# Optimization experiments

Hardware: AMD Instinct MI355X
Metric: run time of the kernel (lower is better)

## Reference

```python
import jax, jax.numpy as jnp
import numpy as np

C = 1024
D = C // 8      # query/key channels
R = C // 16     # channel-attention reduction
B, H, W = 4, 64, 64


def setup_inputs() -> dict:
    key = jax.random.key(0)
    ks = jax.random.split(key, 10)
    s = lambda k, shp, fan: jax.random.normal(k, shp, jnp.float32) * (1.0 / np.sqrt(fan))
    return {
        "x": jax.random.normal(ks[0], (B, C, H, W), jnp.float32),
        "x1": jax.random.normal(ks[1], (B, C, H, W), jnp.float32),
        "Wq": s(ks[2], (D, C), C), "bq": jnp.zeros((D,), jnp.float32),
        "Wk": s(ks[3], (D, C), C), "bk": jnp.zeros((D,), jnp.float32),
        "Wv": s(ks[4], (C, C), C), "bv": jnp.zeros((C,), jnp.float32),
        "Wca1": s(ks[5], (R, C), C),  # CBAM MLP, no bias
        "Wca2": s(ks[6], (C, R), R),
    }


def _forward(x, x1, Wq, bq, Wk, bk, Wv, bv, Wca1, Wca2):
    b, c, h, w = x.shape
    n = h * w
    # 1x1 convs as channel matmuls
    Q = (jnp.einsum('bchw,dc->bdhw', x, Wq) + bq[:, None, None]).reshape(b, D, n)   # [B,D,N]
    K = (jnp.einsum('bchw,dc->bdhw', x, Wk) + bk[:, None, None]).reshape(b, D, n)   # [B,D,N]
    V = (jnp.einsum('bchw,oc->bohw', x1, Wv) + bv[:, None, None]).reshape(b, c, n)  # [B,C,N]
    # energy[b,n,m] = Q[:,n] . K[:,m]
    energy = jnp.einsum('bdn,bdm->bnm', Q, K)
    att = jax.nn.sigmoid(energy)                       # [B,N,N]
    # torch: bmm(V, att^T) -> out[b,c,n] = sum_m V[b,c,m] * att[b,n,m]
    out = jnp.einsum('bcm,bnm->bcn', V, att).reshape(b, c, h, w)
    # ChannelAttention (CBAM): shared MLP on avg+max pooled features, sigmoid gate
    avg = out.mean(axis=(2, 3))                        # [B,C]
    mx = out.max(axis=(2, 3))                          # [B,C]
    mlp = lambda v: jnp.einsum('cr,br->bc', Wca2, jax.nn.relu(jnp.einsum('rc,bc->br', Wca1, v)))
    gate = jax.nn.sigmoid(mlp(avg) + mlp(mx))          # [B,C]
    return out * gate[:, :, None, None]


def reference(x, x1, Wq, bq, Wk, bk, Wv, bv, Wca1, Wca2):
    return _forward(x, x1, Wq, bq, Wk, bk, Wv, bv, Wca1, Wca2)
```

## Files before the change

### kernel.cpp

```cpp
#include <hip/hip_runtime.h>
#include <hip/hip_fp16.h>
#include <cstdint>

typedef _Float16 f16;
typedef __attribute__((ext_vector_type(8))) _Float16 half8;
typedef __attribute__((ext_vector_type(4))) float floatx4;
typedef __attribute__((ext_vector_type(16))) float floatx16;

#define CC 1024
#define DD 128
#define RRR 64
#define BBATCH 4
#define NNN 4096

#define BM 128
#define BN 128
#define BK 64

__device__ __forceinline__ void gl_lds16(const void* g, void* l) {
  __builtin_amdgcn_global_load_lds(
      (__attribute__((address_space(1))) void*)(uintptr_t)g,
      (__attribute__((address_space(3))) void*)l, 16, 0, 0);
}

template<int EPI>
__global__ __launch_bounds__(256)
void gemm_bt(const f16* __restrict__ A, const f16* __restrict__ Bp, f16* __restrict__ Cout,
             const float* __restrict__ bias, int N, int K,
             int lda, int ldb, int ldc, size_t sA, size_t sB, size_t sC)
{
  __shared__ __align__(16) f16 S[2 * BM * BK];
  f16* As = S;
  f16* Bs = S + BM * BK;

  const int z = blockIdx.z;
  const int tid  = threadIdx.x;
  const int lane = tid & 63;
  const int wave = tid >> 6;
  const int m0 = blockIdx.y * BM;
  const int n0 = blockIdx.x * BN;
  const int wm = (wave >> 1) * 64;
  const int wn = (wave & 1) * 64;
  const int l31 = lane & 31;
  const int hi  = lane >> 5;
  const int rs  = lane & 7;

  const f16* Ab = A  + (size_t)z * sA + (size_t)m0 * lda;
  const f16* Bb = Bp + (size_t)z * sB + (size_t)n0 * ldb;

  floatx16 acc[2][2];
#pragma unroll
  for (int i = 0; i < 2; ++i)
#pragma unroll
    for (int j = 0; j < 2; ++j)
#pragma unroll
      for (int r = 0; r < 16; ++r)
        acc[i][j][r] = 0.f;

  int srow[4], ssrc[4];
#pragma unroll
  for (int r = 0; r < 4; ++r) {
    const int gi = r * 256 + tid;
    const int row = gi >> 3;
    const int gc  = gi & 7;
    srow[r] = row;
    ssrc[r] = ((gc ^ (row & 7)) << 3);
  }

  for (int k0 = 0; k0 < K; k0 += BK) {
#pragma unroll
    for (int r = 0; r < 4; ++r) {
      gl_lds16(Ab + (size_t)srow[r] * lda + k0 + ssrc[r], As + (size_t)(r * 256 + tid) * 8);
      gl_lds16(Bb + (size_t)srow[r] * ldb + k0 + ssrc[r], Bs + (size_t)(r * 256 + tid) * 8);
    }
    __syncthreads();

#pragma unroll
    for (int kk = 0; kk < BK; kk += 16) {
      const int gr = (((kk >> 3) + hi) ^ rs) << 3;
      half8 af[2], bfr[2];
#pragma unroll
      for (int i = 0; i < 2; ++i)
        af[i] = *(const half8*)(As + (wm + i * 32 + l31) * BK + gr);
#pragma unroll
      for (int j = 0; j < 2; ++j)
        bfr[j] = *(const half8*)(Bs + (wn + j * 32 + l31) * BK + gr);
#pragma unroll
      for (int i = 0; i < 2; ++i)
#pragma unroll
        for (int j = 0; j < 2; ++j)
          acc[i][j] = __builtin_amdgcn_mfma_f32_32x32x16_f16(af[i], bfr[j], acc[i][j], 0, 0, 0);
    }
    __syncthreads();
  }

  f16* Ch = Cout + (size_t)z * sC;
  f16* Ct = S;
#pragma unroll
  for (int i = 0; i < 2; ++i)
#pragma unroll
    for (int j = 0; j < 2; ++j)
#pragma unroll
      for (int r = 0; r < 16; ++r) {
        const int rl = wm + i * 32 + (r & 3) + 8 * (r >> 2) + 4 * hi;
        const int cl = wn + j * 32 + l31;
        const float v = acc[i][j][r];
        f16 h;
        if constexpr (EPI == 0)      h = (f16)v;
        else if constexpr (EPI == 1) h = (f16)(v + bias[m0 + rl]);
        else if constexpr (EPI == 2) h = (f16)(v + bias[n0 + cl]);
        else                         h = (f16)(1.0f / (1.0f + __expf(-v)));
        Ct[rl * BN + ((((cl >> 3) ^ (rl & 7)) << 3) | (cl & 7))] = h;
      }
  __syncthreads();
#pragma unroll
  for (int p = 0; p < 8; ++p) {
    const int idx = p * 256 + tid;
    const int rl = idx >> 4;
    const int g  = idx & 15;
    half8 vv = *(const half8*)(Ct + rl * BN + ((g ^ (rl & 7)) << 3));
    *(half8*)(Ch + (size_t)(m0 + rl) * ldc + n0 + g * 8) = vv;
  }
}

#define G8_STAGE(MATG, MIDX, LD, H, KT, BUF) do {                                   \
    gl_lds16(MATG + (size_t)((H) * 128 + srow) * (LD) + (KT) * 64 + soff,           \
             &S[BUF][MIDX][(H) * 8192 + tid * 8]);                                  \
    gl_lds16(MATG + (size_t)((H) * 128 + 64 + srow) * (LD) + (KT) * 64 + soff,      \
             &S[BUF][MIDX][(H) * 8192 + 4096 + tid * 8]);                           \
  } while (0)

#define G8_LDA(DST, MA) do {                                                        \
    _Pragma("unroll") for (int ms = 0; ms < 4; ++ms)                                \
    _Pragma("unroll") for (int ks = 0; ks < 2; ++ks)                                \
      DST[ms * 2 + ks] = *(const half8*)(Ac + aRow + (MA) * 4096 + ms * 1024 + sws[ks]); \
  } while (0)

#define G8_LDB(NH) do {                                                             \
    _Pragma("unroll") for (int ns = 0; ns < 2; ++ns)                                \
    _Pragma("unroll") for (int ks = 0; ks < 2; ++ks)                                \
      bf[NH][ns * 2 + ks] = *(const half8*)(Bc + bRow + (NH) * 2048 + ns * 1024 + sws[ks]); \
  } while (0)

#define G8_MFMA(SRC, MA, NH) do {                                                   \
    __builtin_amdgcn_s_setprio(1);                                                  \
    _Pragma("unroll") for (int ms = 0; ms < 4; ++ms)                                \
    _Pragma("unroll") for (int ns = 0; ns < 2; ++ns)                                \
    _Pragma("unroll") for (int ks = 0; ks < 2; ++ks)                                \
      acc[(MA) * 4 + ms][(NH) * 2 + ns] = __builtin_amdgcn_mfma_f32_16x16x32_f16(   \
          SRC[ms * 2 + ks], bf[NH][ns * 2 + ks], acc[(MA) * 4 + ms][(NH) * 2 + ns], 0, 0, 0); \
    __builtin_amdgcn_s_setprio(0);                                                  \
  } while (0)

template<int EPI>
__global__ __launch_bounds__(512, 2)
void gemm8p(const f16* __restrict__ A, const f16* __restrict__ Bp, f16* __restrict__ Cout,
            const float* __restrict__ bias, int K,
            int lda, int ldb, int ldc, size_t sA, size_t sB, size_t sC)
{
  __shared__ __align__(16) f16 S[2][2][16384];

  const int tid  = threadIdx.x;
  const int lane = tid & 63;
  const int wave = tid >> 6;
  const int wm   = wave >> 2;
  const int wn   = wave & 3;
  const int l15  = lane & 15;
  const int lk   = lane >> 4;
  const int z    = blockIdx.z;
  const int m0   = blockIdx.y * 256;
  const int n0   = blockIdx.x * 256;

  const f16* Ag = A  + (size_t)z * sA + (size_t)m0 * lda;
  const f16* Bg = Bp + (size_t)z * sB + (size_t)n0 * ldb;

  const int srow = tid >> 3;
  const int soff = (((tid & 7) ^ (srow & 7)) << 3);

  int sws[2];
#pragma unroll
  for (int ks = 0; ks < 2; ++ks) sws[ks] = (((ks * 4 + lk) ^ (l15 & 7)) << 3);
  const int aRow = (wm * 128 + l15) * 64;
  const int bRow = (wn * 64 + l15) * 64;

  floatx4 acc[8][4];
#pragma unroll
  for (int i = 0; i < 8; ++i)
#pragma unroll
    for (int j = 0; j < 4; ++j)
#pragma unroll
      for (int r = 0; r < 4; ++r) acc[i][j][r] = 0.f;

  half8 af[8], a2[8], bf[2][4];

  const int NT = K >> 6;

  G8_STAGE(Ag, 0, lda, 0, 0, 0);
  G8_STAGE(Bg, 1, ldb, 0, 0, 0);
  G8_STAGE(Ag, 0, lda, 1, 0, 0);
  G8_STAGE(Bg, 1, ldb, 1, 0, 0);
  if (NT > 1) {
    G8_STAGE(Ag, 0, lda, 0, 1, 1);
    G8_STAGE(Bg, 1, ldb, 0, 1, 1);
    G8_STAGE(Ag, 0, lda, 1, 1, 1);
    G8_STAGE(Bg, 1, ldb, 1, 1, 1);
    asm volatile("s_waitcnt vmcnt(8)" ::: "memory");
  } else {
    asm volatile("s_waitcnt vmcnt(0)" ::: "memory");
  }
  __builtin_amdgcn_s_barrier();
  __builtin_amdgcn_sched_barrier(0);

  for (int t = 0; t < NT; ++t) {
    const int cur = t & 1;
    const f16* Ac = &S[cur][0][0];
    const f16* Bc = &S[cur][1][0];

    G8_LDA(af, 0); G8_LDB(0); G8_LDB(1);
    G8_MFMA(af, 0, 0);
    G8_LDA(a2, 1);
    G8_MFMA(af, 0, 1);
    G8_MFMA(a2, 1, 1);
    G8_MFMA(a2, 1, 0);

    asm volatile("s_waitcnt lgkmcnt(0)" ::: "memory");
    __builtin_amdgcn_s_barrier();
    __builtin_amdgcn_sched_barrier(0);

    if (t + 2 < NT) {
      G8_STAGE(Ag, 0, lda, 0, t + 2, cur);
      G8_STAGE(Bg, 1, ldb, 0, t + 2, cur);
      G8_STAGE(Ag, 0, lda, 1, t + 2, cur);
      G8_STAGE(Bg, 1, ldb, 1, t + 2, cur);
      asm volatile("s_waitcnt vmcnt(8)" ::: "memory");
      __builtin_amdgcn_s_barrier();
      __builtin_amdgcn_sched_barrier(0);
    } else if (t + 1 < NT) {
      asm volatile("s_waitcnt vmcnt(0)" ::: "memory");
      __builtin_amdgcn_s_barrier();
      __builtin_amdgcn_sched_barrier(0);
    }
  }

  f16* Ct = &S[0][0][0];
  f16* Ch = Cout + (size_t)z * sC;
#pragma unroll
  for (int mi = 0; mi < 8; ++mi)
#pragma unroll
    for (int ni = 0; ni < 4; ++ni)
#pragma unroll
      for (int r = 0; r < 4; ++r) {
        const int rl = wm * 128 + mi * 16 + lk * 4 + r;
        const int cl = wn * 64 + ni * 16 + l15;
        const float v = acc[mi][ni][r];
        f16 h;
        if constexpr (EPI == 1)      h = (f16)(v + bias[m0 + rl]);
        else if constexpr (EPI == 3) h = (f16)(1.0f / (1.0f + __expf(-v)));
        else                         h = (f16)v;
        Ct[rl * 256 + ((((cl >> 3) ^ (rl & 7)) << 3) | (cl & 7))] = h;
      }
  asm volatile("s_waitcnt lgkmcnt(0)" ::: "memory");
  __builtin_amdgcn_s_barrier();
#pragma unroll
  for (int p = 0; p < 16; ++p) {
    const int idx = p * 512 + tid;
    const int rl = idx >> 5;
    const int g  = idx & 31;
    half8 vv = *(const half8*)(Ct + rl * 256 + ((g ^ (rl & 7)) << 3));
    *(half8*)(Ch + (size_t)(m0 + rl) * ldc + n0 + g * 8) = vv;
  }
}

#undef G8_STAGE
#undef G8_LDA
#undef G8_LDB
#undef G8_MFMA

__global__ __launch_bounds__(256)
void prep(const float* __restrict__ Wq, const float* __restrict__ Wk, const float* __restrict__ Wv,
          const float* __restrict__ bq, const float* __restrict__ bk,
          f16* __restrict__ WQKb, f16* __restrict__ Wvb, float* __restrict__ bqk)
{
  const int NV = CC * CC;
  const int NQ = DD * CC;
  int i = blockIdx.x * 256 + threadIdx.x;
  if (i < NV)                    Wvb[i] = (f16)Wv[i];
  else if (i < NV + NQ)          WQKb[i - NV] = (f16)Wq[i - NV];
  else if (i < NV + 2 * NQ)      WQKb[i - NV] = (f16)Wk[i - NV - NQ];
  else if (i < NV + 2 * NQ + 2 * DD) {
    int t = i - NV - 2 * NQ;
    bqk[t] = (t < DD) ? bq[t] : bk[t - DD];
  }
}

__global__ __launch_bounds__(256)
void transpose_cvt(const float* __restrict__ x, const float* __restrict__ x1,
                   f16* __restrict__ ox, f16* __restrict__ ox1, int nb)
{
  const int zz = blockIdx.z;
  const int b  = (zz < nb) ? zz : zz - nb;
  const float* in = ((zz < nb) ? x : x1) + (size_t)b * CC * NNN;
  f16* out = ((zz < nb) ? ox : ox1) + (size_t)b * CC * NNN;
  __shared__ float tile[64][65];
  const int c0 = blockIdx.y * 64;
  const int n0 = blockIdx.x * 64;
  const int t  = threadIdx.x;
  const int rn = (t & 15) * 4;
  const int rc = t >> 4;
#pragma unroll
  for (int r = 0; r < 4; ++r) {
    const float4 v = *(const float4*)(in + (size_t)(c0 + rc + r * 16) * NNN + n0 + rn);
    tile[rc + r * 16][rn]     = v.x;
    tile[rc + r * 16][rn + 1] = v.y;
    tile[rc + r * 16][rn + 2] = v.z;
    tile[rc + r * 16][rn + 3] = v.w;
  }
  __syncthreads();
  const int ce = (t & 7) * 8;
  const int nr = t >> 3;
#pragma unroll
  for (int r = 0; r < 2; ++r) {
    half8 vv;
#pragma unroll
    for (int e = 0; e < 8; ++e) vv[e] = (f16)tile[ce + e][nr + r * 32];
    *(half8*)(out + (size_t)(n0 + nr + r * 32) * CC + c0 + ce) = vv;
  }
}

__global__ __launch_bounds__(256)
void rowreduce(const f16* __restrict__ X, float* __restrict__ avg, float* __restrict__ mx, int ncols)
{
  const size_t ridx = (size_t)blockIdx.y * gridDim.x + blockIdx.x;
  const half8* p = (const half8*)(X + ridx * ncols);
  float s = 0.f, m = -3.402823466e38f;
  for (int i = threadIdx.x; i < ncols / 8; i += 256) {
    half8 v = p[i];
#pragma unroll
    for (int e = 0; e < 8; ++e) {
      float f = (float)v[e];
      s += f;
      m = fmaxf(m, f);
    }
  }
#pragma unroll
  for (int o = 32; o > 0; o >>= 1) {
    s += __shfl_down(s, o);
    m = fmaxf(m, __shfl_down(m, o));
  }
  __shared__ float ss[4], sm[4];
  if ((threadIdx.x & 63) == 0) { ss[threadIdx.x >> 6] = s; sm[threadIdx.x >> 6] = m; }
  __syncthreads();
  if (threadIdx.x == 0) {
    s = ss[0] + ss[1] + ss[2] + ss[3];
    m = fmaxf(fmaxf(sm[0], sm[1]), fmaxf(sm[2], sm[3]));
    avg[ridx] = s / (float)ncols;
    mx[ridx] = m;
  }
}

__global__ __launch_bounds__(256)
void mlp_gate(const float* __restrict__ avg, const float* __restrict__ mxv,
              const float* __restrict__ W1, const float* __restrict__ W2,
              float* __restrict__ gate)
{
  const int z = blockIdx.x;
  avg += (size_t)z * CC; mxv += (size_t)z * CC; gate += (size_t)z * CC;
  const int t = threadIdx.x;
  const int r = t & 63;
  const int part = t >> 6;
  __shared__ float pa[4][64], pm[4][64], h[RRR];
  {
    const float* w = W1 + (size_t)r * CC + part * 256;
    const float* av = avg + part * 256;
    const float* mv = mxv + part * 256;
    float sa = 0.f, sm = 0.f;
    for (int c = 0; c < 256; ++c) { float wv = w[c]; sa += wv * av[c]; sm += wv * mv[c]; }
    pa[part][r] = sa; pm[part][r] = sm;
  }
  __syncthreads();
  if (t < RRR) {
    float A_ = pa[0][t] + pa[1][t] + pa[2][t] + pa[3][t];
    float M_ = pm[0][t] + pm[1][t] + pm[2][t] + pm[3][t];
    h[t] = fmaxf(A_, 0.f) + fmaxf(M_, 0.f);
  }
  __syncthreads();
  for (int c = t; c < CC; c += 256) {
    float s = 0.f;
    for (int rr = 0; rr < RRR; ++rr) s += W2[(size_t)c * RRR + rr] * h[rr];
    gate[c] = 1.0f / (1.0f + __expf(-s));
  }
}

__global__ __launch_bounds__(256)
void scale_out(const f16* __restrict__ oh, float* __restrict__ out, const float* __restrict__ gate)
{
  oh  += (size_t)blockIdx.y * CC * NNN;
  out += (size_t)blockIdx.y * CC * NNN;
  gate += (size_t)blockIdx.y * CC;
  size_t i = (size_t)blockIdx.x * 256 + threadIdx.x;
  half8 v = ((const half8*)oh)[i];
  const float g = gate[(i * 8) >> 12];
  float4 a = { (float)v[0] * g, (float)v[1] * g, (float)v[2] * g, (float)v[3] * g };
  float4 b = { (float)v[4] * g, (float)v[5] * g, (float)v[6] * g, (float)v[7] * g };
  float4* o = (float4*)out;
  o[2 * i]     = a;
  o[2 * i + 1] = b;
}

extern "C" void kernel_launch(void* const* d_in, const int* in_sizes, int n_in,
                              void* d_out, int out_size, void* d_ws, size_t ws_size,
                              hipStream_t stream)
{
  const float* x    = (const float*)d_in[0];
  const float* x1   = (const float*)d_in[1];
  const float* Wq   = (const float*)d_in[2];
  const float* bq   = (const float*)d_in[3];
  const float* Wk   = (const float*)d_in[4];
  const float* bk   = (const float*)d_in[5];
  const float* Wv   = (const float*)d_in[6];
  const float* bv   = (const float*)d_in[7];
  const float* Wca1 = (const float*)d_in[8];
  const float* Wca2 = (const float*)d_in[9];
  float* out = (float*)d_out;

  char* ws = (char*)d_ws;
  size_t off = 0;
  auto alloc = [&](size_t bytes) { void* p = ws + off; off += (bytes + 255) & ~255ULL; return p; };

  f16* WQKb = (f16*)alloc((size_t)2 * DD * CC * 2);
  f16* Wvb  = (f16*)alloc((size_t)CC * CC * 2);
  float* bqk  = (float*)alloc(256 * 4);
  float* avg  = (float*)alloc((size_t)BBATCH * CC * 4);
  float* mxv  = (float*)alloc((size_t)BBATCH * CC * 4);
  float* gate = (float*)alloc((size_t)BBATCH * CC * 4);

  const size_t attB = (size_t)NNN * NNN * 2;
  const size_t xTB  = (size_t)BBATCH * NNN * CC * 2;
  const size_t qkB  = (size_t)BBATCH * NNN * 2 * DD * 2;
  const size_t vBB  = (size_t)BBATCH * CC * NNN * 2;
  const size_t ohB  = (size_t)BBATCH * CC * NNN * 2;
  const size_t fixedEnd = off;

  const dim3 blk(256);
  const int prepN = CC * CC + 2 * DD * CC + 2 * DD;
  prep<<<(prepN + 255) / 256, blk, 0, stream>>>(Wq, Wk, Wv, bq, bk, WQKb, Wvb, bqk);

  {
    size_t offF = fixedEnd;
    auto af_ = [&](size_t bytes) { void* p = ws + offF; offF += (bytes + 255) & ~255ULL; return p; };
    f16* QKt  = (f16*)af_(qkB);
    f16* Vb   = (f16*)af_(vBB);
    f16* outh = (f16*)af_(ohB);
    f16* att  = (f16*)af_((size_t)BBATCH * attB);
    if (offF + (1 << 20) <= ws_size) {
      f16* xTb  = att;
      f16* x1Tb = att + (size_t)BBATCH * NNN * CC;

      transpose_cvt<<<dim3(NNN / 64, CC / 64, 2 * BBATCH), blk, 0, stream>>>(x, x1, xTb, x1Tb, BBATCH);

      gemm_bt<2><<<dim3(2 * DD / BN, NNN / BM, BBATCH), blk, 0, stream>>>(
          xTb, WQKb, QKt, bqk, 2 * DD, CC,
          CC, CC, 2 * DD, (size_t)NNN * CC, 0, (size_t)NNN * 2 * DD);
      gemm8p<1><<<dim3(NNN / 256, CC / 256, BBATCH), dim3(512), 0, stream>>>(
          Wvb, x1Tb, Vb, bv, CC,
          CC, CC, NNN, 0, (size_t)NNN * CC, (size_t)CC * NNN);

      const size_t sQK = (size_t)NNN * 2 * DD;
      gemm8p<3><<<dim3(NNN / 256, NNN / 256, BBATCH), dim3(512), 0, stream>>>(
          QKt, QKt + DD, att, nullptr, DD,
          2 * DD, 2 * DD, NNN, sQK, sQK, (size_t)NNN * NNN);
      gemm8p<0><<<dim3(NNN / 256, CC / 256, BBATCH), dim3(512), 0, stream>>>(
          Vb, att, outh, nullptr, NNN,
          NNN, NNN, NNN, (size_t)CC * NNN, (size_t)NNN * NNN, (size_t)CC * NNN);

      rowreduce<<<dim3(CC, BBATCH), blk, 0, stream>>>(outh, avg, mxv, NNN);
      mlp_gate<<<BBATCH, blk, 0, stream>>>(avg, mxv, Wca1, Wca2, gate);
      scale_out<<<dim3(CC * NNN / 8 / 256, BBATCH), blk, 0, stream>>>(outh, out, gate);
      return;
    }
  }

  int g = 0;
  for (int cand = BBATCH; cand >= 1; cand >>= 1) {
    size_t need = fixedEnd + 2 * xTB + qkB + vBB + ohB + (size_t)cand * attB + (1 << 20);
    if (need <= ws_size) { g = cand; break; }
  }

  if (g > 0) {
    f16* xTb  = (f16*)alloc(xTB);
    f16* x1Tb = (f16*)alloc(xTB);
    f16* QKt  = (f16*)alloc(qkB);
    f16* Vb   = (f16*)alloc(vBB);
    f16* outh = (f16*)alloc(ohB);
    f16* att  = (f16*)alloc((size_t)g * attB);

    transpose_cvt<<<dim3(NNN / 64, CC / 64, 2 * BBATCH), blk, 0, stream>>>(x, x1, xTb, x1Tb, BBATCH);

    gemm_bt<2><<<dim3(2 * DD / BN, NNN / BM, BBATCH), blk, 0, stream>>>(
        xTb, WQKb, QKt, bqk, 2 * DD, CC,
        CC, CC, 2 * DD, (size_t)NNN * CC, 0, (size_t)NNN * 2 * DD);
    gemm_bt<1><<<dim3(NNN / BN, CC / BM, BBATCH), blk, 0, stream>>>(
        Wvb, x1Tb, Vb, bv, NNN, CC,
        CC, CC, NNN, 0, (size_t)NNN * CC, (size_t)CC * NNN);

    for (int b0 = 0; b0 < BBATCH; b0 += g) {
      const int gc = (b0 + g <= BBATCH) ? g : (BBATCH - b0);
      const size_t sQK = (size_t)NNN * 2 * DD;
      gemm_bt<3><<<dim3(NNN / BN, NNN / BM, gc), blk, 0, stream>>>(
          QKt + (size_t)b0 * sQK, QKt + (size_t)b0 * sQK + DD, att, nullptr,
          NNN, DD, 2 * DD, 2 * DD, NNN, sQK, sQK, (size_t)NNN * NNN);
      gemm_bt<0><<<dim3(NNN / BN, CC / BM, gc), blk, 0, stream>>>(
          Vb + (size_t)b0 * CC * NNN, att, outh + (size_t)b0 * CC * NNN, nullptr,
          NNN, NNN, NNN, NNN, NNN,
          (size_t)CC * NNN, (size_t)NNN * NNN, (size_t)CC * NNN);
    }

    rowreduce<<<dim3(CC, BBATCH), blk, 0, stream>>>(outh, avg, mxv, NNN);
    mlp_gate<<<BBATCH, blk, 0, stream>>>(avg, mxv, Wca1, Wca2, gate);
    scale_out<<<dim3(CC * NNN / 8 / 256, BBATCH), blk, 0, stream>>>(outh, out, gate);
  } else {
    f16* xTb  = (f16*)alloc((size_t)NNN * CC * 2);
    f16* x1Tb = (f16*)alloc((size_t)NNN * CC * 2);
    f16* QKt  = (f16*)alloc((size_t)NNN * 2 * DD * 2);
    f16* Vb   = (f16*)alloc((size_t)CC * NNN * 2);
    f16* outh = (f16*)alloc((size_t)CC * NNN * 2);
    f16* att  = (f16*)alloc(attB);

    for (int b = 0; b < BBATCH; ++b) {
      const float* xb  = x  + (size_t)b * CC * NNN;
      const float* x1b = x1 + (size_t)b * CC * NNN;
      float* outb = out + (size_t)b * CC * NNN;

      transpose_cvt<<<dim3(NNN / 64, CC / 64, 2), blk, 0, stream>>>(xb, x1b, xTb, x1Tb, 1);

      gemm_bt<2><<<dim3(2 * DD / BN, NNN / BM, 1), blk, 0, stream>>>(
          xTb, WQKb, QKt, bqk, 2 * DD, CC, CC, CC, 2 * DD, 0, 0, 0);
      gemm_bt<1><<<dim3(NNN / BN, CC / BM, 1), blk, 0, stream>>>(
          Wvb, x1Tb, Vb, bv, NNN, CC, CC, CC, NNN, 0, 0, 0);
      gemm_bt<3><<<dim3(NNN / BN, NNN / BM, 1), blk, 0, stream>>>(
          QKt, QKt + DD, att, nullptr, NNN, DD, 2 * DD, 2 * DD, NNN, 0, 0, 0);
      gemm_bt<0><<<dim3(NNN / BN, CC / BM, 1), blk, 0, stream>>>(
          Vb, att, outh, nullptr, NNN, NNN, NNN, NNN, NNN, 0, 0, 0);

      rowreduce<<<dim3(CC, 1), blk, 0, stream>>>(outh, avg + (size_t)b * CC, mxv + (size_t)b * CC, NNN);
      mlp_gate<<<1, blk, 0, stream>>>(avg + (size_t)b * CC, mxv + (size_t)b * CC, Wca1, Wca2, gate + (size_t)b * CC);
      scale_out<<<dim3(CC * NNN / 8 / 256, 1), blk, 0, stream>>>(outh, outb, gate + (size_t)b * CC);
    }
  }
}
```

Measured before the change: 475.6 us.

## Fuse channel avg/max pooling into output GEMM epilogue and prefetch LDS fragments

The final attention-output GEMM now computes per-row sums and maxima from its fp32 accumulators and merges them with global atomicAdd and an order-preserving-integer atomicMax. This removes the separate rowreduce pass over the fp16 output. The prep kernel zero-initialises the accumulators, and mlp_gate decodes the max and divides the sum by N. The GEMM main loop also loads the first A/B fragments for the next tile before the loop iteration, and leading dimensions become compile-time template constants. The costs are atomic contention on the stats, pooling taken from fp32 accumulators instead of the rounded fp16 values, and extra register pressure from the prefetch.

```diff
diff --git a/kernel.cpp b/kernel.cpp
--- a/kernel.cpp
+++ b/kernel.cpp
@@ -123,23 +123,23 @@
   }
 }
 
-#define G8_STAGE(MATG, MIDX, LD, H, KT, BUF) do {                                   \
+#define G8_STAGE(MATG, LD, MIDX, H, KT, BUF) do {                                   \
     gl_lds16(MATG + (size_t)((H) * 128 + srow) * (LD) + (KT) * 64 + soff,           \
              &S[BUF][MIDX][(H) * 8192 + tid * 8]);                                  \
     gl_lds16(MATG + (size_t)((H) * 128 + 64 + srow) * (LD) + (KT) * 64 + soff,      \
              &S[BUF][MIDX][(H) * 8192 + 4096 + tid * 8]);                           \
   } while (0)
 
-#define G8_LDA(DST, MA) do {                                                        \
+#define G8_LDA(BASE, DST, MA) do {                                                  \
     _Pragma("unroll") for (int ms = 0; ms < 4; ++ms)                                \
     _Pragma("unroll") for (int ks = 0; ks < 2; ++ks)                                \
-      DST[ms * 2 + ks] = *(const half8*)(Ac + aRow + (MA) * 4096 + ms * 1024 + sws[ks]); \
+      DST[ms * 2 + ks] = *(const half8*)((BASE) + aRow + (MA) * 4096 + ms * 1024 + sws[ks]); \
   } while (0)
 
-#define G8_LDB(NH) do {                                                             \
+#define G8_LDB(BASE, NH) do {                                                       \
     _Pragma("unroll") for (int ns = 0; ns < 2; ++ns)                                \
     _Pragma("unroll") for (int ks = 0; ks < 2; ++ks)                                \
-      bf[NH][ns * 2 + ks] = *(const half8*)(Bc + bRow + (NH) * 2048 + ns * 1024 + sws[ks]); \
+      bf[NH][ns * 2 + ks] = *(const half8*)((BASE) + bRow + (NH) * 2048 + ns * 1024 + sws[ks]); \
   } while (0)
 
 #define G8_MFMA(SRC, MA, NH) do {                                                   \
@@ -152,11 +152,11 @@
     __builtin_amdgcn_s_setprio(0);                                                  \
   } while (0)
 
-template<int EPI>
+template<int EPI, int LDA, int LDB, bool STATS>
 __global__ __launch_bounds__(512, 2)
 void gemm8p(const f16* __restrict__ A, const f16* __restrict__ Bp, f16* __restrict__ Cout,
-            const float* __restrict__ bias, int K,
-            int lda, int ldb, int ldc, size_t sA, size_t sB, size_t sC)
+            const float* __restrict__ bias, float* __restrict__ avgp, unsigned* __restrict__ mxp,
+            int K, int ldc, size_t sA, size_t sB, size_t sC)
 {
   __shared__ __align__(16) f16 S[2][2][16384];
 
@@ -171,8 +171,8 @@
   const int m0   = blockIdx.y * 256;
   const int n0   = blockIdx.x * 256;
 
-  const f16* Ag = A  + (size_t)z * sA + (size_t)m0 * lda;
-  const f16* Bg = Bp + (size_t)z * sB + (size_t)n0 * ldb;
+  const f16* Ag = A  + (size_t)z * sA + (size_t)m0 * LDA;
+  const f16* Bg = Bp + (size_t)z * sB + (size_t)n0 * LDB;
 
   const int srow = tid >> 3;
   const int soff = (((tid & 7) ^ (srow & 7)) << 3);
@@ -195,30 +195,32 @@
 
   const int NT = K >> 6;
 
-  G8_STAGE(Ag, 0, lda, 0, 0, 0);
-  G8_STAGE(Bg, 1, ldb, 0, 0, 0);
-  G8_STAGE(Ag, 0, lda, 1, 0, 0);
-  G8_STAGE(Bg, 1, ldb, 1, 0, 0);
+  G8_STAGE(Ag, LDA, 0, 0, 0, 0);
+  G8_STAGE(Bg, LDB, 1, 0, 0, 0);
+  G8_STAGE(Ag, LDA, 0, 1, 0, 0);
+  G8_STAGE(Bg, LDB, 1, 1, 0, 0);
   if (NT > 1) {
-    G8_STAGE(Ag, 0, lda, 0, 1, 1);
-    G8_STAGE(Bg, 1, ldb, 0, 1, 1);
-    G8_STAGE(Ag, 0, lda, 1, 1, 1);
-    G8_STAGE(Bg, 1, ldb, 1, 1, 1);
+    G8_STAGE(Ag, LDA, 0, 0, 1, 1);
+    G8_STAGE(Bg, LDB, 1, 0, 1, 1);
+    G8_STAGE(Ag, LDA, 0, 1, 1, 1);
+    G8_STAGE(Bg, LDB, 1, 1, 1, 1);
     asm volatile("s_waitcnt vmcnt(8)" ::: "memory");
   } else {
     asm volatile("s_waitcnt vmcnt(0)" ::: "memory");
   }
   __builtin_amdgcn_s_barrier();
   __builtin_amdgcn_sched_barrier(0);
+  G8_LDA((&S[0][0][0]), af, 0);
+  G8_LDB((&S[0][1][0]), 0);
 
   for (int t = 0; t < NT; ++t) {
-    const int cur = t & 1;
+    const int cur = t & 1, nxt = cur ^ 1;
     const f16* Ac = &S[cur][0][0];
     const f16* Bc = &S[cur][1][0];
 
-    G8_LDA(af, 0); G8_LDB(0); G8_LDB(1);
+    G8_LDB(Bc, 1);
+    G8_LDA(Ac, a2, 1);
     G8_MFMA(af, 0, 0);
-    G8_LDA(a2, 1);
     G8_MFMA(af, 0, 1);
     G8_MFMA(a2, 1, 1);
     G8_MFMA(a2, 1, 0);
@@ -228,20 +230,46 @@
     __builtin_amdgcn_sched_barrier(0);
 
     if (t + 2 < NT) {
-      G8_STAGE(Ag, 0, lda, 0, t + 2, cur);
-      G8_STAGE(Bg, 1, ldb, 0, t + 2, cur);
-      G8_STAGE(Ag, 0, lda, 1, t + 2, cur);
-      G8_STAGE(Bg, 1, ldb, 1, t + 2, cur);
+      G8_STAGE(Ag, LDA, 0, 0, t + 2, cur);
+      G8_STAGE(Bg, LDB, 1, 0, t + 2, cur);
+      G8_STAGE(Ag, LDA, 0, 1, t + 2, cur);
+      G8_STAGE(Bg, LDB, 1, 1, t + 2, cur);
       asm volatile("s_waitcnt vmcnt(8)" ::: "memory");
+    } else if (t + 1 < NT) {
+      asm volatile("s_waitcnt vmcnt(0)" ::: "memory");
+    }
+    if (t + 1 < NT) {
       __builtin_amdgcn_s_barrier();
       __builtin_amdgcn_sched_barrier(0);
-    } else if (t + 1 < NT) {
-      asm volatile("s_waitcnt vmcnt(0)" ::: "memory");
-      __builtin_amdgcn_s_barrier();
-      __builtin_amdgcn_sched_barrier(0);
-    }
-  }
-
+      G8_LDA((&S[nxt][0][0]), af, 0);
+      G8_LDB((&S[nxt][1][0]), 0);
+    }
+  }
+
+  if constexpr (STATS) {
+#pragma unroll
+    for (int mi = 0; mi < 8; ++mi)
+#pragma unroll
+      for (int r = 0; r < 4; ++r) {
+        float s  = acc[mi][0][r] + acc[mi][1][r] + acc[mi][2][r] + acc[mi][3][r];
+        float mv = fmaxf(fmaxf(acc[mi][0][r], acc[mi][1][r]), fmaxf(acc[mi][2][r], acc[mi][3][r]));
+#pragma unroll
+        for (int o = 1; o < 16; o <<= 1) {
+          s += __shfl_xor(s, o);
+          mv = fmaxf(mv, __shfl_xor(mv, o));
+        }
+        if (l15 == 0) {
+          const int row = z * CC + m0 + wm * 128 + mi * 16 + lk * 4 + r;
+          atomicAdd(avgp + row, s);
+          unsigned bits = __float_as_uint(mv);
+          unsigned u = (bits & 0x80000000u) ? ~bits : (bits | 0x80000000u);
+          atomicMax(mxp + row, u);
+        }
+      }
+  }
+
+  asm volatile("s_waitcnt lgkmcnt(0)" ::: "memory");
+  __builtin_amdgcn_s_barrier();
   f16* Ct = &S[0][0][0];
   f16* Ch = Cout + (size_t)z * sC;
 #pragma unroll
@@ -279,10 +307,12 @@
 __global__ __launch_bounds__(256)
 void prep(const float* __restrict__ Wq, const float* __restrict__ Wk, const float* __restrict__ Wv,
           const float* __restrict__ bq, const float* __restrict__ bk,
-          f16* __restrict__ WQKb, f16* __restrict__ Wvb, float* __restrict__ bqk)
+          f16* __restrict__ WQKb, f16* __restrict__ Wvb, float* __restrict__ bqk,
+          float* __restrict__ avgz, unsigned* __restrict__ mxz)
 {
   const int NV = CC * CC;
   const int NQ = DD * CC;
+  const int NS = BBATCH * CC;
   int i = blockIdx.x * 256 + threadIdx.x;
   if (i < NV)                    Wvb[i] = (f16)Wv[i];
   else if (i < NV + NQ)          WQKb[i - NV] = (f16)Wq[i - NV];
@@ -290,6 +320,10 @@
   else if (i < NV + 2 * NQ + 2 * DD) {
     int t = i - NV - 2 * NQ;
     bqk[t] = (t < DD) ? bq[t] : bk[t - DD];
+  } else if (i < NV + 2 * NQ + 2 * DD + NS) {
+    avgz[i - NV - 2 * NQ - 2 * DD] = 0.f;
+  } else if (i < NV + 2 * NQ + 2 * DD + 2 * NS) {
+    mxz[i - NV - 2 * NQ - 2 * DD - NS] = 0x007FFFFFu;
   }
 }
 
@@ -358,6 +392,7 @@
   }
 }
 
+template<int MODE>
 __global__ __launch_bounds__(256)
 void mlp_gate(const float* __restrict__ avg, const float* __restrict__ mxv,
               const float* __restrict__ W1, const float* __restrict__ W2,
@@ -374,7 +409,20 @@
     const float* av = avg + part * 256;
     const float* mv = mxv + part * 256;
     float sa = 0.f, sm = 0.f;
-    for (int c = 0; c < 256; ++c) { float wv = w[c]; sa += wv * av[c]; sm += wv * mv[c]; }
+    for (int c = 0; c < 256; ++c) {
+      float wv = w[c];
+      float mval;
+      if constexpr (MODE == 1) {
+        unsigned u = ((const unsigned*)mv)[c];
+        unsigned b = (u & 0x80000000u) ? (u ^ 0x80000000u) : ~u;
+        mval = __uint_as_float(b);
+      } else {
+        mval = mv[c];
+      }
+      sa += wv * av[c];
+      sm += wv * mval;
+    }
+    if constexpr (MODE == 1) sa *= (1.0f / (float)NNN);
     pa[part][r] = sa; pm[part][r] = sm;
   }
   __syncthreads();
@@ -442,8 +490,9 @@
   const size_t fixedEnd = off;
 
   const dim3 blk(256);
-  const int prepN = CC * CC + 2 * DD * CC + 2 * DD;
-  prep<<<(prepN + 255) / 256, blk, 0, stream>>>(Wq, Wk, Wv, bq, bk, WQKb, Wvb, bqk);
+  const int prepN = CC * CC + 2 * DD * CC + 2 * DD + 2 * BBATCH * CC;
+  prep<<<(prepN + 255) / 256, blk, 0, stream>>>(Wq, Wk, Wv, bq, bk, WQKb, Wvb, bqk,
+                                                avg, (unsigned*)mxv);
 
   {
     size_t offF = fixedEnd;
@@ -461,20 +510,19 @@
       gemm_bt<2><<<dim3(2 * DD / BN, NNN / BM, BBATCH), blk, 0, stream>>>(
           xTb, WQKb, QKt, bqk, 2 * DD, CC,
           CC, CC, 2 * DD, (size_t)NNN * CC, 0, (size_t)NNN * 2 * DD);
-      gemm8p<1><<<dim3(NNN / 256, CC / 256, BBATCH), dim3(512), 0, stream>>>(
-          Wvb, x1Tb, Vb, bv, CC,
-          CC, CC, NNN, 0, (size_t)NNN * CC, (size_t)CC * NNN);
+      gemm8p<1, CC, CC, false><<<dim3(NNN / 256, CC / 256, BBATCH), dim3(512), 0, stream>>>(
+          Wvb, x1Tb, Vb, bv, nullptr, nullptr, CC,
+          NNN, 0, (size_t)NNN * CC, (size_t)CC * NNN);
 
       const size_t sQK = (size_t)NNN * 2 * DD;
-      gemm8p<3><<<dim3(NNN / 256, NNN / 256, BBATCH), dim3(512), 0, stream>>>(
-          QKt, QKt + DD, att, nullptr, DD,
-          2 * DD, 2 * DD, NNN, sQK, sQK, (size_t)NNN * NNN);
-      gemm8p<0><<<dim3(NNN / 256, CC / 256, BBATCH), dim3(512), 0, stream>>>(
-          Vb, att, outh, nullptr, NNN,
-          NNN, NNN, NNN, (size_t)CC * NNN, (size_t)NNN * NNN, (size_t)CC * NNN);
-
-      rowreduce<<<dim3(CC, BBATCH), blk, 0, stream>>>(outh, avg, mxv, NNN);
-      mlp_gate<<<BBATCH, blk, 0, stream>>>(avg, mxv, Wca1, Wca2, gate);
+      gemm8p<3, 2 * DD, 2 * DD, false><<<dim3(NNN / 256, NNN / 256, BBATCH), dim3(512), 0, stream>>>(
+          QKt, QKt + DD, att, nullptr, nullptr, nullptr, DD,
+          NNN, sQK, sQK, (size_t)NNN * NNN);
+      gemm8p<0, NNN, NNN, true><<<dim3(NNN / 256, CC / 256, BBATCH), dim3(512), 0, stream>>>(
+          Vb, att, outh, nullptr, avg, (unsigned*)mxv, NNN,
+          NNN, (size_t)CC * NNN, (size_t)NNN * NNN, (size_t)CC * NNN);
+
+      mlp_gate<1><<<BBATCH, blk, 0, stream>>>(avg, mxv, Wca1, Wca2, gate);
       scale_out<<<dim3(CC * NNN / 8 / 256, BBATCH), blk, 0, stream>>>(outh, out, gate);
       return;
     }
@@ -516,7 +564,7 @@
     }
 
     rowreduce<<<dim3(CC, BBATCH), blk, 0, stream>>>(outh, avg, mxv, NNN);
-    mlp_gate<<<BBATCH, blk, 0, stream>>>(avg, mxv, Wca1, Wca2, gate);
+    mlp_gate<0><<<BBATCH, blk, 0, stream>>>(avg, mxv, Wca1, Wca2, gate);
     scale_out<<<dim3(CC * NNN / 8 / 256, BBATCH), blk, 0, stream>>>(outh, out, gate);
   } else {
     f16* xTb  = (f16*)alloc((size_t)NNN * CC * 2);
@@ -543,7 +591,7 @@
           Vb, att, outh, nullptr, NNN, NNN, NNN, NNN, NNN, 0, 0, 0);
 
       rowreduce<<<dim3(CC, 1), blk, 0, stream>>>(outh, avg + (size_t)b * CC, mxv + (size_t)b * CC, NNN);
-      mlp_gate<<<1, blk, 0, stream>>>(avg + (size_t)b * CC, mxv + (size_t)b * CC, Wca1, Wca2, gate + (size_t)b * CC);
+      mlp_gate<0><<<1, blk, 0, stream>>>(avg + (size_t)b * CC, mxv + (size_t)b * CC, Wca1, Wca2, gate + (size_t)b * CC);
       scale_out<<<dim3(CC * NNN / 8 / 256, 1), blk, 0, stream>>>(outh, outb, gate + (size_t)b * CC);
     }
   }
```

Result: slower. 487.3 us (+2.5%).
